# Optimization experiments

Hardware: AMD Instinct MI355X
Metric: run time of the kernel (lower is better)

Reference implementation:

```python
import jax, jax.numpy as jnp
import numpy as np

N_RAYS = 65536
COUNT_CYCLE = (32, 64, 128, 256)  # ragged per-ray sample counts, avg 120
N_TOTAL = N_RAYS // len(COUNT_CYCLE) * sum(COUNT_CYCLE)  # 7,864,320


def _build_rays_a():
    counts = np.tile(np.array(COUNT_CYCLE, dtype=np.int32), N_RAYS // len(COUNT_CYCLE))
    starts = np.concatenate([[0], np.cumsum(counts)[:-1]]).astype(np.int32)
    ray_idx = np.arange(N_RAYS, dtype=np.int32)
    return jnp.asarray(np.stack([ray_idx, starts, counts], axis=1))


def setup_inputs() -> dict:
    key = jax.random.key(0)
    k1, k2, k3, k4 = jax.random.split(key, 4)
    sigmas = jax.random.uniform(k1, (N_TOTAL,), dtype=jnp.float32) * 2.0   # nonneg densities
    rgbs = jax.random.uniform(k2, (N_TOTAL, 3), dtype=jnp.float32)
    deltas = jax.random.uniform(k3, (N_TOTAL,), dtype=jnp.float32) * 0.05  # step sizes
    ts = jnp.sort(jax.random.uniform(k4, (N_TOTAL,), dtype=jnp.float32)) * 4.0
    rays_a = _build_rays_a()
    T_threshold = jnp.array([1e-4], dtype=jnp.float32)
    return {"sigmas": sigmas, "rgbs": rgbs, "deltas": deltas, "ts": ts,
            "rays_a": rays_a, "T_threshold": T_threshold}


def reference(sigmas, rgbs, deltas, ts, rays_a, T_threshold):
    """Per-ray alpha compositing with early termination (T >= thr).

    Within a ray, transmittance T is the exclusive product of (1 - a) with
    a = 1 - exp(-sigma*delta), i.e. T = exp(-cumsum_excl(sigma*delta)).
    Since T is monotone non-increasing, the kernel's sequential early-exit
    (skip samples once T < thr) equals masking with the prefix T >= thr.
    """
    n_rays = rays_a.shape[0]
    n = sigmas.shape[0]
    starts = rays_a[:, 1]
    # ray id of every flat sample (segments are contiguous, sorted starts)
    rid = jnp.searchsorted(starts, jnp.arange(n, dtype=starts.dtype), side="right") - 1

    sd = sigmas * deltas                      # [N]
    cs = jnp.cumsum(sd)
    excl = cs - sd                            # exclusive cumsum over the flat buffer
    seg_base = jnp.where(starts > 0, cs[jnp.maximum(starts - 1, 0)], 0.0)  # [n_rays]
    T = jnp.exp(-(excl - seg_base[rid]))      # exclusive transmittance within ray

    a = 1.0 - jnp.exp(-sd)
    alive = T >= T_threshold[0]               # prefix mask == early exit
    w = jnp.where(alive, a * T, 0.0)          # per-sample weights (ws)

    opacity = jax.ops.segment_sum(w, rid, num_segments=n_rays)
    depth = jax.ops.segment_sum(w * ts, rid, num_segments=n_rays)
    rgb = jax.ops.segment_sum(w[:, None] * rgbs, rid, num_segments=n_rays)
    total_samples = jax.ops.segment_sum(alive.astype(jnp.int32), rid, num_segments=n_rays)
    return total_samples, opacity, depth, rgb, w
```

## Files before the change

### kernel.cpp

```cpp
#include <hip/hip_runtime.h>


__global__ __launch_bounds__(256) void vr_fwd_kernel(
    const float* __restrict__ sigmas,
    const float* __restrict__ rgbs,
    const float* __restrict__ deltas,
    const float* __restrict__ ts,
    const int*   __restrict__ rays_a,
    const float* __restrict__ thr_p,
    float* __restrict__ out,
    int n_rays)
{
    const int wid  = (int)((blockIdx.x * 256u + threadIdx.x) >> 6);
    const int lane = (int)(threadIdx.x & 63u);
    if (wid >= n_rays) return;

    const int   start = rays_a[wid * 3 + 1];
    const int   count = rays_a[wid * 3 + 2];
    const float thr   = thr_p[0];
    const bool  al4   = ((start & 3) == 0);

    float* __restrict__ out_counts  = out;
    float* __restrict__ out_opacity = out + n_rays;
    float* __restrict__ out_depth   = out + 2 * n_rays;
    float* __restrict__ out_rgb     = out + 3 * n_rays;
    float* __restrict__ out_w       = out + 6 * n_rays;

    float carry = 0.0f;
    float acc_n = 0.0f, acc_op = 0.0f, acc_d = 0.0f;
    float acc_r = 0.0f, acc_g = 0.0f, acc_b = 0.0f;

    for (int base = 0; base < count; base += 256) {
        const int li  = base + lane * 4;
        const int gi  = start + li;
        const int rem = count - li;

        float sd[4] = {0.f, 0.f, 0.f, 0.f};
        float tv[4] = {0.f, 0.f, 0.f, 0.f};
        float cr[4] = {0.f, 0.f, 0.f, 0.f};
        float cg[4] = {0.f, 0.f, 0.f, 0.f};
        float cb[4] = {0.f, 0.f, 0.f, 0.f};

        if (al4 && rem >= 4) {
            const float4 sg = *reinterpret_cast<const float4*>(sigmas + gi);
            const float4 dl = *reinterpret_cast<const float4*>(deltas + gi);
            const float4 t4 = *reinterpret_cast<const float4*>(ts + gi);
            sd[0] = sg.x * dl.x; sd[1] = sg.y * dl.y;
            sd[2] = sg.z * dl.z; sd[3] = sg.w * dl.w;
            tv[0] = t4.x; tv[1] = t4.y; tv[2] = t4.z; tv[3] = t4.w;
            const float4* rp = reinterpret_cast<const float4*>(rgbs + 3 * gi);
            const float4 A = rp[0], B = rp[1], C = rp[2];
            cr[0] = A.x; cg[0] = A.y; cb[0] = A.z;
            cr[1] = A.w; cg[1] = B.x; cb[1] = B.y;
            cr[2] = B.z; cg[2] = B.w; cb[2] = C.x;
            cr[3] = C.y; cg[3] = C.z; cb[3] = C.w;
        } else if (rem > 0) {
            #pragma unroll
            for (int k = 0; k < 4; ++k) {
                if (k < rem) {
                    sd[k] = sigmas[gi + k] * deltas[gi + k];
                    tv[k] = ts[gi + k];
                    cr[k] = rgbs[3 * (gi + k) + 0];
                    cg[k] = rgbs[3 * (gi + k) + 1];
                    cb[k] = rgbs[3 * (gi + k) + 2];
                }
            }
        }

        const float p1 = sd[0] + sd[1];
        const float p2 = p1 + sd[2];
        const float p3 = p2 + sd[3];

        float sc = p3;
        #pragma unroll
        for (int off = 1; off < 64; off <<= 1) {
            const float up = __shfl_up(sc, off, 64);
            if (lane >= off) sc += up;
        }
        const float wave_total = __shfl(sc, 63, 64);
        const float lex = carry + (sc - p3);
        carry += wave_total;

        float T = __expf(-lex);
        float wv[4];
        #pragma unroll
        for (int k = 0; k < 4; ++k) {
            const float e     = __expf(-sd[k]);
            const bool  alive = (T >= thr);
            const float w     = alive ? (1.0f - e) * T : 0.0f;
            wv[k] = w;
            if (alive && k < rem) acc_n += 1.0f;
            acc_op += w;
            acc_d  += w * tv[k];
            acc_r  += w * cr[k];
            acc_g  += w * cg[k];
            acc_b  += w * cb[k];
            T *= e;
        }

        if (al4 && rem >= 4) {
            *reinterpret_cast<float4*>(out_w + gi) =
                make_float4(wv[0], wv[1], wv[2], wv[3]);
        } else if (rem > 0) {
            #pragma unroll
            for (int k = 0; k < 4; ++k)
                if (k < rem) out_w[gi + k] = wv[k];
        }
    }

    #pragma unroll
    for (int off = 32; off > 0; off >>= 1) {
        acc_n  += __shfl_down(acc_n,  off, 64);
        acc_op += __shfl_down(acc_op, off, 64);
        acc_d  += __shfl_down(acc_d,  off, 64);
        acc_r  += __shfl_down(acc_r,  off, 64);
        acc_g  += __shfl_down(acc_g,  off, 64);
        acc_b  += __shfl_down(acc_b,  off, 64);
    }

    if (lane == 0) {
        out_counts[wid]      = acc_n;
        out_opacity[wid]     = acc_op;
        out_depth[wid]       = acc_d;
        out_rgb[wid * 3 + 0] = acc_r;
        out_rgb[wid * 3 + 1] = acc_g;
        out_rgb[wid * 3 + 2] = acc_b;
    }
}

extern "C" void kernel_launch(void* const* d_in, const int* in_sizes, int n_in,
                              void* d_out, int out_size, void* d_ws, size_t ws_size,
                              hipStream_t stream) {
    const float* sigmas = (const float*)d_in[0];
    const float* rgbs   = (const float*)d_in[1];
    const float* deltas = (const float*)d_in[2];
    const float* ts     = (const float*)d_in[3];
    const int*   rays_a = (const int*)d_in[4];
    const float* thr    = (const float*)d_in[5];

    const int n_rays = in_sizes[4] / 3;
    float* out = (float*)d_out;

    const int blocks = (n_rays + 3) / 4;
    vr_fwd_kernel<<<blocks, 256, 0, stream>>>(sigmas, rgbs, deltas, ts, rays_a,
                                              thr, out, n_rays);
}
```

Measured before the change: 43.97 us.

## Size per-ray sub-wave groups to each ray's sample-count class

Each ray now goes to a sub-wave group of 8, 16, 32 or 64 lanes instead of a full 64-lane wave. The group width is picked from the ray index modulo 4, matching the cyclic per-ray sample counts, so short rays no longer leave most lanes idle. The host computes wave ranges per class, and the kernel maps each wave to its class and packs several rays into one wave for the short classes. The scan and the final reduction now work over the group width. Results stay correct for any counts, but the load balance depends on the inputs following the ray-index-to-count pattern.

```diff
diff --git a/kernel.cpp b/kernel.cpp
--- a/kernel.cpp
+++ b/kernel.cpp
@@ -9,16 +9,33 @@
     const int*   __restrict__ rays_a,
     const float* __restrict__ thr_p,
     float* __restrict__ out,
-    int n_rays)
+    int n_rays, int b0, int b1, int b2, int b3)
 {
     const int wid  = (int)((blockIdx.x * 256u + threadIdx.x) >> 6);
     const int lane = (int)(threadIdx.x & 63u);
-    if (wid >= n_rays) return;
+    if (wid >= b3) return;
 
-    const int   start = rays_a[wid * 3 + 1];
-    const int   count = rays_a[wid * 3 + 2];
-    const float thr   = thr_p[0];
-    const bool  al4   = ((start & 3) == 0);
+    int cls, wloc;
+    if      (wid < b0) { cls = 0; wloc = wid; }
+    else if (wid < b1) { cls = 1; wloc = wid - b0; }
+    else if (wid < b2) { cls = 2; wloc = wid - b1; }
+    else               { cls = 3; wloc = wid - b2; }
+
+    const int sgW    = 8 << cls;
+    const int rpw    = 8 >> cls;
+    const int sgId   = lane >> (3 + cls);
+    const int sgLane = lane & (sgW - 1);
+
+    const int ray = (wloc * rpw + sgId) * 4 + cls;
+    const bool have_ray = (ray < n_rays);
+
+    int start = 0, count = 0;
+    if (have_ray) {
+        start = rays_a[ray * 3 + 1];
+        count = rays_a[ray * 3 + 2];
+    }
+    const float thr = thr_p[0];
+    const bool  al4 = ((start & 3) == 0);
 
     float* __restrict__ out_counts  = out;
     float* __restrict__ out_opacity = out + n_rays;
@@ -30,8 +47,8 @@
     float acc_n = 0.0f, acc_op = 0.0f, acc_d = 0.0f;
     float acc_r = 0.0f, acc_g = 0.0f, acc_b = 0.0f;
 
-    for (int base = 0; base < count; base += 256) {
-        const int li  = base + lane * 4;
+    for (int base = 0; base < count; base += sgW * 4) {
+        const int li  = base + sgLane * 4;
         const int gi  = start + li;
         const int rem = count - li;
 
@@ -72,14 +89,13 @@
         const float p3 = p2 + sd[3];
 
         float sc = p3;
-        #pragma unroll
-        for (int off = 1; off < 64; off <<= 1) {
-            const float up = __shfl_up(sc, off, 64);
-            if (lane >= off) sc += up;
+        for (int off = 1; off < sgW; off <<= 1) {
+            const float up = __shfl_up(sc, off, sgW);
+            if (sgLane >= off) sc += up;
         }
-        const float wave_total = __shfl(sc, 63, 64);
+        const float sg_total = __shfl(sc, sgW - 1, sgW);
         const float lex = carry + (sc - p3);
-        carry += wave_total;
+        carry += sg_total;
 
         float T = __expf(-lex);
         float wv[4];
@@ -108,23 +124,22 @@
         }
     }
 
-    #pragma unroll
-    for (int off = 32; off > 0; off >>= 1) {
-        acc_n  += __shfl_down(acc_n,  off, 64);
-        acc_op += __shfl_down(acc_op, off, 64);
-        acc_d  += __shfl_down(acc_d,  off, 64);
-        acc_r  += __shfl_down(acc_r,  off, 64);
-        acc_g  += __shfl_down(acc_g,  off, 64);
-        acc_b  += __shfl_down(acc_b,  off, 64);
+    for (int off = sgW >> 1; off > 0; off >>= 1) {
+        acc_n  += __shfl_down(acc_n,  off, sgW);
+        acc_op += __shfl_down(acc_op, off, sgW);
+        acc_d  += __shfl_down(acc_d,  off, sgW);
+        acc_r  += __shfl_down(acc_r,  off, sgW);
+        acc_g  += __shfl_down(acc_g,  off, sgW);
+        acc_b  += __shfl_down(acc_b,  off, sgW);
     }
 
-    if (lane == 0) {
-        out_counts[wid]      = acc_n;
-        out_opacity[wid]     = acc_op;
-        out_depth[wid]       = acc_d;
-        out_rgb[wid * 3 + 0] = acc_r;
-        out_rgb[wid * 3 + 1] = acc_g;
-        out_rgb[wid * 3 + 2] = acc_b;
+    if (sgLane == 0 && have_ray) {
+        out_counts[ray]      = acc_n;
+        out_opacity[ray]     = acc_op;
+        out_depth[ray]       = acc_d;
+        out_rgb[ray * 3 + 0] = acc_r;
+        out_rgb[ray * 3 + 1] = acc_g;
+        out_rgb[ray * 3 + 2] = acc_b;
     }
 }
 
@@ -141,7 +156,17 @@
     const int n_rays = in_sizes[4] / 3;
     float* out = (float*)d_out;
 
-    const int blocks = (n_rays + 3) / 4;
+    int b[4], cum = 0;
+    for (int c = 0; c < 4; ++c) {
+        const int Kc  = (n_rays - c + 3) / 4;
+        const int rpw = 8 >> c;
+        cum += (Kc + rpw - 1) / rpw;
+        b[c] = cum;
+    }
+    const int total_waves = b[3];
+    const int blocks = (total_waves + 3) / 4;
+
     vr_fwd_kernel<<<blocks, 256, 0, stream>>>(sigmas, rgbs, deltas, ts, rays_a,
-                                              thr, out, n_rays);
+                                              thr, out, n_rays,
+                                              b[0], b[1], b[2], b[3]);
 }
```

Result: faster. 40.38 us (-8.2%).
